# Kernel optimization log

Measured on AMD Instinct MI355X. Metric: run time of the kernel, lower is better.

Reference implementation:

```python
import jax, jax.numpy as jnp
import numpy as np

FIELD_DIMS = [256] * 8          # 8 fields, 2048 total features
N_FACTORS = 64
BATCH = 8192
INIT_STD = 0.01


def setup_inputs() -> dict:
    key = jax.random.key(0)
    k_x, k_v = jax.random.split(key)
    n_features = sum(FIELD_DIMS)
    n_fields = len(FIELD_DIMS)
    x = jax.random.normal(k_x, (BATCH, n_features), dtype=jnp.float32)
    # Parameters initialized as in FFMtorchNN.initialize()
    b = jnp.zeros((1,), dtype=jnp.float32)
    w = jnp.zeros((n_features, 1), dtype=jnp.float32)
    V = INIT_STD * jax.random.normal(k_v, (n_features, n_fields, N_FACTORS), dtype=jnp.float32)
    # feat2field[i] = field index of feature i
    feat2field = jnp.asarray(np.repeat(np.arange(n_fields), FIELD_DIMS), dtype=jnp.int32)
    return {"x": x, "b": b, "w": w, "V": V, "feat2field": feat2field}


def reference(x, b, w, V, feat2field):
    # Linear term: sum(x @ w, dim=1) -> [B]
    total_linear = (x @ w)[:, 0]

    n_fields = V.shape[1]
    # One-hot field membership of each feature: E [F, n_fields]
    E = jax.nn.one_hot(feat2field, n_fields, dtype=x.dtype)
    # M[b, s, t, l] = sum_{i in field s} x[b,i] * V[i, t, l]
    M = jnp.einsum('bi,is,itl->bstl', x, E, V)

    # Full ordered-pair bilinear sum: sum_{i,j} x_i x_j <V[i, f(j)], V[j, f(i)]>
    full = jnp.einsum('bstl,btsl->b', M, M)
    # Self terms (i == j): x_i^2 * ||V[i, f(i)]||^2
    V_self = jnp.take_along_axis(V, feat2field[:, None, None].astype(jnp.int32), axis=1)[:, 0, :]  # [F, L]
    q = jnp.einsum('bi,i->b', x * x, jnp.sum(V_self * V_self, axis=-1))

    # Original: total_inter = sum_{i<j} 0.5 * <t_i, t_j>  ==  0.25 * (full - q)
    total_inter = 0.25 * (full - q)

    y_pred = b[0] + total_linear + total_inter  # [B]
    return y_pred
```

## Files before the change

kernel.cpp:

```cpp
#include <hip/hip_runtime.h>

#define BATCH  8192
#define NFEAT  2048
#define NFIELD 8
#define NFACT  64
#define FDIM   256
#define NPAIR  36

typedef short short8v __attribute__((ext_vector_type(8)));
typedef __bf16 bf16x8 __attribute__((ext_vector_type(8)));
typedef float f32x4 __attribute__((ext_vector_type(4)));

__device__ inline unsigned short f2bf(float f) {
    unsigned int u = __float_as_uint(f);
    unsigned int r = u + 0x7FFF + ((u >> 16) & 1);
    return (unsigned short)(r >> 16);
}
__device__ inline float bf2f(unsigned short h) {
    return __uint_as_float(((unsigned int)h) << 16);
}
__device__ inline f32x4 mfma16(bf16x8 a, bf16x8 b, f32x4 c) {
    return __builtin_amdgcn_mfma_f32_16x16x32_bf16(a, b, c, 0, 0, 0);
}

__global__ void sv_kernel(const float* __restrict__ V, const int* __restrict__ f2f,
                          float* __restrict__ sv) {
    int i = blockIdx.x * blockDim.x + threadIdx.x;
    if (i >= NFEAT) return;
    int f = f2f[i];
    const float* vp = V + (size_t)i * (NFIELD * NFACT) + (size_t)f * NFACT;
    float s = 0.f;
#pragma unroll
    for (int l = 0; l < NFACT; l += 4) {
        float4 v = *reinterpret_cast<const float4*>(vp + l);
        s += v.x * v.x + v.y * v.y + v.z * v.z + v.w * v.w;
    }
    sv[i] = s;
}

__global__ void init_out(const float* __restrict__ bptr, float* __restrict__ out) {
    int i = blockIdx.x * blockDim.x + threadIdx.x;
    if (i < BATCH) out[i] = bptr[0];
}

__global__ void convert_v(const float* __restrict__ V,
                          unsigned short* __restrict__ vh, unsigned short* __restrict__ vl) {
    const int tid = blockIdx.x * 256 + threadIdx.x;
    const int lane = tid & 63;
    const int ct = (tid >> 6) & 3;
    const int kc = (tid >> 8) & 7;
    const int t  = (tid >> 11) & 7;
    const int s  = tid >> 14;
    const int l  = ct * 16 + (lane & 15);
    const int i0 = s * 256 + kc * 32 + (lane >> 4) * 8;
    short8v hv, lv;
#pragma unroll
    for (int e = 0; e < 8; ++e) {
        float v = V[(size_t)(i0 + e) * (NFIELD * NFACT) + t * NFACT + l];
        unsigned short h = f2bf(v);
        hv[e] = (short)h;
        lv[e] = (short)f2bf(v - bf2f(h));
    }
    *reinterpret_cast<short8v*>(vh + (size_t)tid * 8) = hv;
    *reinterpret_cast<short8v*>(vl + (size_t)tid * 8) = lv;
}

__global__ __launch_bounds__(256) void convert_x3(
    const float* __restrict__ x, const float* __restrict__ w,
    const float* __restrict__ sv,
    unsigned short* __restrict__ xh, unsigned short* __restrict__ xl,
    float* __restrict__ out) {
    __shared__ float tile[16][260];

    const int bid = blockIdx.x;
    const int rb  = bid >> 6;
    const int rt  = (bid >> 3) & 7;
    const int s   = bid & 7;
    const int row0 = rb * 128 + rt * 16;

    const int tid  = threadIdx.x;
    const int lane = tid & 63;
    const int wv   = tid >> 6;

    const int col = s * 256 + lane * 4;
    float4 w4  = *reinterpret_cast<const float4*>(w + col);
    float4 sv4 = *reinterpret_cast<const float4*>(sv + col);

    float lq[4];
#pragma unroll
    for (int p = 0; p < 4; ++p) {
        const int r = wv * 4 + p;
        float4 v = *reinterpret_cast<const float4*>(
            x + (size_t)(row0 + r) * NFEAT + col);
        *reinterpret_cast<float4*>(&tile[r][lane * 4]) = v;
        float lin = v.x * w4.x + v.y * w4.y + v.z * w4.z + v.w * w4.w;
        float q   = v.x * v.x * sv4.x + v.y * v.y * sv4.y
                  + v.z * v.z * sv4.z + v.w * v.w * sv4.w;
        lq[p] = lin - 0.25f * q;
    }
#pragma unroll
    for (int off = 1; off < 64; off <<= 1)
#pragma unroll
        for (int p = 0; p < 4; ++p)
            lq[p] += __shfl_xor(lq[p], off, 64);
    if (lane == 0) {
#pragma unroll
        for (int p = 0; p < 4; ++p)
            atomicAdd(&out[row0 + wv * 4 + p], lq[p]);
    }

    __syncthreads();

#pragma unroll
    for (int half = 0; half < 2; ++half) {
        const int kc = half * 4 + wv;
        const int r  = lane & 15;
        const int k0 = kc * 32 + (lane >> 4) * 8;
        float4 a = *reinterpret_cast<const float4*>(&tile[r][k0]);
        float4 b = *reinterpret_cast<const float4*>(&tile[r][k0 + 4]);
        float vs[8] = {a.x, a.y, a.z, a.w, b.x, b.y, b.z, b.w};
        short8v hv, lv;
#pragma unroll
        for (int e = 0; e < 8; ++e) {
            unsigned short h = f2bf(vs[e]);
            hv[e] = (short)h;
            lv[e] = (short)f2bf(vs[e] - bf2f(h));
        }
        size_t off = ((((size_t)(rb * 8 + s) * 8 + kc) * 8 + rt) * 64 + lane) * 8;
        *reinterpret_cast<short8v*>(xh + off) = hv;
        *reinterpret_cast<short8v*>(xl + off) = lv;
    }
}

__global__ __launch_bounds__(256, 3) void pair_mfma3(
    const unsigned short* __restrict__ xh, const unsigned short* __restrict__ xl,
    const unsigned short* __restrict__ vh, const unsigned short* __restrict__ vl,
    float* __restrict__ out) {
    __shared__ unsigned short lds[24576];

    const int id    = blockIdx.x;
    const int local = id >> 3;
    const int tile  = (id & 7) * 8 + local / 36;
    int p = local % 36;
    int s = 0;
    while (p >= NFIELD - s) { p -= NFIELD - s; ++s; }
    const int t = s + p;
    const bool diag = (s == t);

    const int tid = threadIdx.x, lane = tid & 63, wid = tid >> 6;
    const int rt0 = wid * 2, rt1 = rt0 + 1;

    f32x4 accA[2][4] = {};
    f32x4 accB[2][4] = {};

    const unsigned short* xsrc = (wid & 1) ? xl : xh;
    const unsigned short* vsrc = (wid & 1) ? vl : vh;
    const int f     = (wid < 2) ? s : t;
    const int vpair = (wid < 2) ? (s * 8 + t) : (t * 8 + s);
    const int xdst  = wid * 4096;
    const int vdst  = 16384 + wid * 2048;
    const bool active = !(diag && wid >= 2);

    const size_t xbase = ((size_t)(tile * 8 + f) * 8) * 4096 + (size_t)lane * 8;
    const size_t vbase = ((size_t)(vpair * 8)) * 2048 + (size_t)lane * 8;

    short8v xr[8], vr[4];
    if (active) {
#pragma unroll
        for (int rt = 0; rt < 8; ++rt)
            xr[rt] = *reinterpret_cast<const short8v*>(xsrc + xbase + rt * 512);
#pragma unroll
        for (int ct = 0; ct < 4; ++ct)
            vr[ct] = *reinterpret_cast<const short8v*>(vsrc + vbase + ct * 512);
    }

    for (int kc = 0; kc < 8; ++kc) {
        __syncthreads();
        if (active) {
#pragma unroll
            for (int rt = 0; rt < 8; ++rt)
                *reinterpret_cast<short8v*>(&lds[xdst + rt * 512 + lane * 8]) = xr[rt];
#pragma unroll
            for (int ct = 0; ct < 4; ++ct)
                *reinterpret_cast<short8v*>(&lds[vdst + ct * 512 + lane * 8]) = vr[ct];
        }
        __syncthreads();

        if (kc < 7 && active) {
            const size_t xo = xbase + (size_t)(kc + 1) * 4096;
            const size_t vo = vbase + (size_t)(kc + 1) * 2048;
#pragma unroll
            for (int rt = 0; rt < 8; ++rt)
                xr[rt] = *reinterpret_cast<const short8v*>(xsrc + xo + rt * 512);
#pragma unroll
            for (int ct = 0; ct < 4; ++ct)
                vr[ct] = *reinterpret_cast<const short8v*>(vsrc + vo + ct * 512);
        }

        bf16x8 ah0 = *reinterpret_cast<const bf16x8*>(&lds[0     + rt0 * 512 + lane * 8]);
        bf16x8 ah1 = *reinterpret_cast<const bf16x8*>(&lds[0     + rt1 * 512 + lane * 8]);
        bf16x8 al0 = *reinterpret_cast<const bf16x8*>(&lds[4096  + rt0 * 512 + lane * 8]);
        bf16x8 al1 = *reinterpret_cast<const bf16x8*>(&lds[4096  + rt1 * 512 + lane * 8]);
#pragma unroll
        for (int ct = 0; ct < 4; ++ct) {
            bf16x8 bh = *reinterpret_cast<const bf16x8*>(&lds[16384 + ct * 512 + lane * 8]);
            bf16x8 bl = *reinterpret_cast<const bf16x8*>(&lds[18432 + ct * 512 + lane * 8]);
            accA[0][ct] = mfma16(ah0, bh, accA[0][ct]);
            accA[0][ct] = mfma16(ah0, bl, accA[0][ct]);
            accA[0][ct] = mfma16(al0, bh, accA[0][ct]);
            accA[1][ct] = mfma16(ah1, bh, accA[1][ct]);
            accA[1][ct] = mfma16(ah1, bl, accA[1][ct]);
            accA[1][ct] = mfma16(al1, bh, accA[1][ct]);
        }
        if (!diag) {
            bf16x8 ch0 = *reinterpret_cast<const bf16x8*>(&lds[8192  + rt0 * 512 + lane * 8]);
            bf16x8 ch1 = *reinterpret_cast<const bf16x8*>(&lds[8192  + rt1 * 512 + lane * 8]);
            bf16x8 cl0 = *reinterpret_cast<const bf16x8*>(&lds[12288 + rt0 * 512 + lane * 8]);
            bf16x8 cl1 = *reinterpret_cast<const bf16x8*>(&lds[12288 + rt1 * 512 + lane * 8]);
#pragma unroll
            for (int ct = 0; ct < 4; ++ct) {
                bf16x8 bh = *reinterpret_cast<const bf16x8*>(&lds[20480 + ct * 512 + lane * 8]);
                bf16x8 bl = *reinterpret_cast<const bf16x8*>(&lds[22528 + ct * 512 + lane * 8]);
                accB[0][ct] = mfma16(ch0, bh, accB[0][ct]);
                accB[0][ct] = mfma16(ch0, bl, accB[0][ct]);
                accB[0][ct] = mfma16(cl0, bh, accB[0][ct]);
                accB[1][ct] = mfma16(ch1, bh, accB[1][ct]);
                accB[1][ct] = mfma16(ch1, bl, accB[1][ct]);
                accB[1][ct] = mfma16(cl1, bh, accB[1][ct]);
            }
        }
    }

    const float scale = diag ? 0.25f : 0.5f;
#pragma unroll
    for (int rti = 0; rti < 2; ++rti) {
#pragma unroll
        for (int r = 0; r < 4; ++r) {
            float v = 0.f;
#pragma unroll
            for (int ct = 0; ct < 4; ++ct)
                v += accA[rti][ct][r] * (diag ? accA[rti][ct][r] : accB[rti][ct][r]);
            v += __shfl_xor(v, 1, 64);
            v += __shfl_xor(v, 2, 64);
            v += __shfl_xor(v, 4, 64);
            v += __shfl_xor(v, 8, 64);
            if ((lane & 15) == 0) {
                int row = tile * 128 + (wid * 2 + rti) * 16 + (lane >> 4) * 4 + r;
                atomicAdd(&out[row], scale * v);
            }
        }
    }
}

#define BM 64
#define KC 64
#define XPAD 4

__global__ void base_kernel(const float* __restrict__ x, const float* __restrict__ bptr,
                            const float* __restrict__ w, const float* __restrict__ sv,
                            float* __restrict__ out) {
    const int row = blockIdx.x;
    const int tid = threadIdx.x;
    const float* xr = x + (size_t)row * NFEAT;
    float lin = 0.f, q = 0.f;
#pragma unroll
    for (int j = 0; j < 2; ++j) {
        int idx = j * 1024 + tid * 4;
        float4 xv = *reinterpret_cast<const float4*>(xr + idx);
        float4 wv = *reinterpret_cast<const float4*>(w + idx);
        float4 sq = *reinterpret_cast<const float4*>(sv + idx);
        lin += xv.x * wv.x + xv.y * wv.y + xv.z * wv.z + xv.w * wv.w;
        q   += xv.x * xv.x * sq.x + xv.y * xv.y * sq.y
             + xv.z * xv.z * sq.z + xv.w * xv.w * sq.w;
    }
#pragma unroll
    for (int off = 32; off >= 1; off >>= 1) {
        lin += __shfl_down(lin, off, 64);
        q   += __shfl_down(q, off, 64);
    }
    __shared__ float slin[4], sq4[4];
    const int wave = tid >> 6;
    if ((tid & 63) == 0) { slin[wave] = lin; sq4[wave] = q; }
    __syncthreads();
    if (tid == 0) {
        float L = slin[0] + slin[1] + slin[2] + slin[3];
        float Q = sq4[0] + sq4[1] + sq4[2] + sq4[3];
        out[row] = bptr[0] + L - 0.25f * Q;
    }
}

__global__ __launch_bounds__(256) void pair_kernel(const float* __restrict__ x,
                                                   const float* __restrict__ V,
                                                   float* __restrict__ out) {
    __shared__ float Xs[BM][KC + XPAD];
    __shared__ float Xt[BM][KC + XPAD];
    __shared__ float Vs[KC][NFACT];
    __shared__ float Vt[KC][NFACT];

    const int tile = blockIdx.x;
    int p = blockIdx.y;
    int s = 0;
    while (p >= NFIELD - s) { p -= NFIELD - s; ++s; }
    const int t = s + p;
    const bool diag = (s == t);

    const int tid  = threadIdx.x;
    const int lgrp = tid & 15;
    const int rgrp = tid >> 4;
    const int l0 = lgrp * 4;
    const int r0 = rgrp * 4;
    const int rowBase = tile * BM;

    float accA[4][4] = {};
    float accB[4][4] = {};

    for (int kc = 0; kc < FDIM; kc += KC) {
        __syncthreads();
#pragma unroll
        for (int it = 0; it < 4; ++it) {
            int rr = (tid >> 4) + it * 16;
            const float* gx = x + (size_t)(rowBase + rr) * NFEAT + s * FDIM + kc + (tid & 15) * 4;
            *reinterpret_cast<float4*>(&Xs[rr][(tid & 15) * 4]) =
                *reinterpret_cast<const float4*>(gx);
            if (!diag) {
                const float* gx2 = x + (size_t)(rowBase + rr) * NFEAT + t * FDIM + kc + (tid & 15) * 4;
                *reinterpret_cast<float4*>(&Xt[rr][(tid & 15) * 4]) =
                    *reinterpret_cast<const float4*>(gx2);
            }
        }
#pragma unroll
        for (int it = 0; it < 4; ++it) {
            int kk = (tid >> 4) + it * 16;
            const float* gv = V + (size_t)(s * FDIM + kc + kk) * (NFIELD * NFACT) + t * NFACT + (tid & 15) * 4;
            *reinterpret_cast<float4*>(&Vs[kk][(tid & 15) * 4]) =
                *reinterpret_cast<const float4*>(gv);
            if (!diag) {
                const float* gv2 = V + (size_t)(t * FDIM + kc + kk) * (NFIELD * NFACT) + s * NFACT + (tid & 15) * 4;
                *reinterpret_cast<float4*>(&Vt[kk][(tid & 15) * 4]) =
                    *reinterpret_cast<const float4*>(gv2);
            }
        }
        __syncthreads();

        for (int k = 0; k < KC; k += 4) {
            float xa[4][4], va[4][4];
#pragma unroll
            for (int r = 0; r < 4; ++r) {
                float4 v = *reinterpret_cast<const float4*>(&Xs[r0 + r][k]);
                xa[r][0] = v.x; xa[r][1] = v.y; xa[r][2] = v.z; xa[r][3] = v.w;
            }
#pragma unroll
            for (int kk = 0; kk < 4; ++kk) {
                float4 v = *reinterpret_cast<const float4*>(&Vs[k + kk][l0]);
                va[kk][0] = v.x; va[kk][1] = v.y; va[kk][2] = v.z; va[kk][3] = v.w;
            }
#pragma unroll
            for (int kk = 0; kk < 4; ++kk)
#pragma unroll
                for (int r = 0; r < 4; ++r)
#pragma unroll
                    for (int c = 0; c < 4; ++c)
                        accA[r][c] = fmaf(xa[r][kk], va[kk][c], accA[r][c]);

            if (!diag) {
                float xb[4][4], vb[4][4];
#pragma unroll
                for (int r = 0; r < 4; ++r) {
                    float4 v = *reinterpret_cast<const float4*>(&Xt[r0 + r][k]);
                    xb[r][0] = v.x; xb[r][1] = v.y; xb[r][2] = v.z; xb[r][3] = v.w;
                }
#pragma unroll
                for (int kk = 0; kk < 4; ++kk) {
                    float4 v = *reinterpret_cast<const float4*>(&Vt[k + kk][l0]);
                    vb[kk][0] = v.x; vb[kk][1] = v.y; vb[kk][2] = v.z; vb[kk][3] = v.w;
                }
#pragma unroll
                for (int kk = 0; kk < 4; ++kk)
#pragma unroll
                    for (int r = 0; r < 4; ++r)
#pragma unroll
                        for (int c = 0; c < 4; ++c)
                            accB[r][c] = fmaf(xb[r][kk], vb[kk][c], accB[r][c]);
            }
        }
    }

    float pr[4];
#pragma unroll
    for (int r = 0; r < 4; ++r) {
        float d = 0.f;
#pragma unroll
        for (int c = 0; c < 4; ++c)
            d += accA[r][c] * (diag ? accA[r][c] : accB[r][c]);
        pr[r] = d;
    }
#pragma unroll
    for (int off = 1; off < 16; off <<= 1) {
#pragma unroll
        for (int r = 0; r < 4; ++r)
            pr[r] += __shfl_xor(pr[r], off, 64);
    }
    if (lgrp == 0) {
        const float scale = diag ? 0.25f : 0.5f;
#pragma unroll
        for (int r = 0; r < 4; ++r)
            atomicAdd(&out[rowBase + r0 + r], scale * pr[r]);
    }
}

extern "C" void kernel_launch(void* const* d_in, const int* in_sizes, int n_in,
                              void* d_out, int out_size, void* d_ws, size_t ws_size,
                              hipStream_t stream) {
    const float* x   = (const float*)d_in[0];
    const float* b   = (const float*)d_in[1];
    const float* w   = (const float*)d_in[2];
    const float* V   = (const float*)d_in[3];
    const int*   f2f = (const int*)d_in[4];
    float* out = (float*)d_out;

    const size_t SZ_XH = 33554432;
    const size_t SZ_VH = 2097152;
    const size_t NEED  = 2 * SZ_XH + 2 * SZ_VH + NFEAT * sizeof(float);

    if (ws_size >= NEED) {
        char* ws = (char*)d_ws;
        unsigned short* xhp = (unsigned short*)ws;
        unsigned short* xlp = (unsigned short*)(ws + SZ_XH);
        unsigned short* vhp = (unsigned short*)(ws + 2 * SZ_XH);
        unsigned short* vlp = (unsigned short*)(ws + 2 * SZ_XH + SZ_VH);
        float* sv = (float*)(ws + 2 * SZ_XH + 2 * SZ_VH);

        sv_kernel<<<(NFEAT + 255) / 256, 256, 0, stream>>>(V, f2f, sv);
        init_out<<<(BATCH + 255) / 256, 256, 0, stream>>>(b, out);
        convert_v<<<131072 / 256, 256, 0, stream>>>(V, vhp, vlp);
        convert_x3<<<4096, 256, 0, stream>>>(x, w, sv, xhp, xlp, out);
        pair_mfma3<<<64 * NPAIR, 256, 0, stream>>>(xhp, xlp, vhp, vlp, out);
    } else {
        float* sv = (float*)d_ws;
        sv_kernel<<<(NFEAT + 255) / 256, 256, 0, stream>>>(V, f2f, sv);
        base_kernel<<<BATCH, 256, 0, stream>>>(x, b, w, sv, out);
        dim3 grid(BATCH / BM, NPAIR);
        pair_kernel<<<grid, 256, 0, stream>>>(x, V, out);
    }
}
```

Baseline: 178.9 us.

## Load X fragments directly into registers and double-buffer only V in LDS

Reworks the pair MFMA kernel so each wave loads its X row fragments (hi/lo) straight from global memory into registers instead of staging them through shared memory, and only the V tiles go through a double-buffered LDS buffer. Waves now split output into a 2x2 grid over row tiles and column tiles rather than taking row tiles only. This cuts LDS traffic and footprint and drops one barrier per k-step. In exchange, X fragments are read from global memory twice (once per column-half wave), register pressure rises, and global load latency is exposed because X is not prefetched.

```diff
diff --git a/kernel.cpp b/kernel.cpp
--- a/kernel.cpp
+++ b/kernel.cpp
@@ -132,11 +132,11 @@
     }
 }
 
-__global__ __launch_bounds__(256, 3) void pair_mfma3(
+__global__ __launch_bounds__(256, 3) void pair_mfma4(
     const unsigned short* __restrict__ xh, const unsigned short* __restrict__ xl,
     const unsigned short* __restrict__ vh, const unsigned short* __restrict__ vl,
     float* __restrict__ out) {
-    __shared__ unsigned short lds[24576];
+    __shared__ unsigned short vbuf[2][4][2048];
 
     const int id    = blockIdx.x;
     const int local = id >> 3;
@@ -148,104 +148,105 @@
     const bool diag = (s == t);
 
     const int tid = threadIdx.x, lane = tid & 63, wid = tid >> 6;
-    const int rt0 = wid * 2, rt1 = rt0 + 1;
-
-    f32x4 accA[2][4] = {};
-    f32x4 accB[2][4] = {};
-
-    const unsigned short* xsrc = (wid & 1) ? xl : xh;
+    const int rh = wid >> 1;
+    const int ch = wid & 1;
+
+    f32x4 accA[4][2] = {};
+    f32x4 accB[4][2] = {};
+
     const unsigned short* vsrc = (wid & 1) ? vl : vh;
-    const int f     = (wid < 2) ? s : t;
     const int vpair = (wid < 2) ? (s * 8 + t) : (t * 8 + s);
-    const int xdst  = wid * 4096;
-    const int vdst  = 16384 + wid * 2048;
-    const bool active = !(diag && wid >= 2);
-
-    const size_t xbase = ((size_t)(tile * 8 + f) * 8) * 4096 + (size_t)lane * 8;
-    const size_t vbase = ((size_t)(vpair * 8)) * 2048 + (size_t)lane * 8;
-
-    short8v xr[8], vr[4];
-    if (active) {
-#pragma unroll
-        for (int rt = 0; rt < 8; ++rt)
-            xr[rt] = *reinterpret_cast<const short8v*>(xsrc + xbase + rt * 512);
-#pragma unroll
-        for (int ct = 0; ct < 4; ++ct)
-            vr[ct] = *reinterpret_cast<const short8v*>(vsrc + vbase + ct * 512);
+    const bool vactive = !(diag && wid >= 2);
+    const size_t vbase = (size_t)vpair * 8 * 2048 + (size_t)(lane * 8);
+
+    const size_t xbaseS = (size_t)(tile * 8 + s) * 8 * 4096
+                        + (size_t)((rh * 4) * 512 + lane * 8);
+    const size_t xbaseT = (size_t)(tile * 8 + t) * 8 * 4096
+                        + (size_t)((rh * 4) * 512 + lane * 8);
+
+    if (vactive) {
+        short8v vr[4];
+#pragma unroll
+        for (int i = 0; i < 4; ++i)
+            vr[i] = *reinterpret_cast<const short8v*>(vsrc + vbase + i * 512);
+#pragma unroll
+        for (int i = 0; i < 4; ++i)
+            *reinterpret_cast<short8v*>(&vbuf[0][wid][i * 512 + lane * 8]) = vr[i];
     }
 
     for (int kc = 0; kc < 8; ++kc) {
+        const int cur = kc & 1;
+        const size_t xoS = xbaseS + (size_t)kc * 4096;
+        const size_t xoT = xbaseT + (size_t)kc * 4096;
+
+        bf16x8 xah[4], xal[4], xch[4], xcl[4];
+#pragma unroll
+        for (int i = 0; i < 4; ++i) {
+            xah[i] = *reinterpret_cast<const bf16x8*>(xh + xoS + i * 512);
+            xal[i] = *reinterpret_cast<const bf16x8*>(xl + xoS + i * 512);
+        }
+        if (!diag) {
+#pragma unroll
+            for (int i = 0; i < 4; ++i) {
+                xch[i] = *reinterpret_cast<const bf16x8*>(xh + xoT + i * 512);
+                xcl[i] = *reinterpret_cast<const bf16x8*>(xl + xoT + i * 512);
+            }
+        }
+        short8v vn[4];
+        if (kc < 7 && vactive) {
+            const size_t vo = vbase + (size_t)(kc + 1) * 2048;
+#pragma unroll
+            for (int i = 0; i < 4; ++i)
+                vn[i] = *reinterpret_cast<const short8v*>(vsrc + vo + i * 512);
+        }
+
         __syncthreads();
-        if (active) {
-#pragma unroll
-            for (int rt = 0; rt < 8; ++rt)
-                *reinterpret_cast<short8v*>(&lds[xdst + rt * 512 + lane * 8]) = xr[rt];
-#pragma unroll
-            for (int ct = 0; ct < 4; ++ct)
-                *reinterpret_cast<short8v*>(&lds[vdst + ct * 512 + lane * 8]) = vr[ct];
-        }
-        __syncthreads();
-
-        if (kc < 7 && active) {
-            const size_t xo = xbase + (size_t)(kc + 1) * 4096;
-            const size_t vo = vbase + (size_t)(kc + 1) * 2048;
-#pragma unroll
-            for (int rt = 0; rt < 8; ++rt)
-                xr[rt] = *reinterpret_cast<const short8v*>(xsrc + xo + rt * 512);
-#pragma unroll
-            for (int ct = 0; ct < 4; ++ct)
-                vr[ct] = *reinterpret_cast<const short8v*>(vsrc + vo + ct * 512);
-        }
-
-        bf16x8 ah0 = *reinterpret_cast<const bf16x8*>(&lds[0     + rt0 * 512 + lane * 8]);
-        bf16x8 ah1 = *reinterpret_cast<const bf16x8*>(&lds[0     + rt1 * 512 + lane * 8]);
-        bf16x8 al0 = *reinterpret_cast<const bf16x8*>(&lds[4096  + rt0 * 512 + lane * 8]);
-        bf16x8 al1 = *reinterpret_cast<const bf16x8*>(&lds[4096  + rt1 * 512 + lane * 8]);
-#pragma unroll
-        for (int ct = 0; ct < 4; ++ct) {
-            bf16x8 bh = *reinterpret_cast<const bf16x8*>(&lds[16384 + ct * 512 + lane * 8]);
-            bf16x8 bl = *reinterpret_cast<const bf16x8*>(&lds[18432 + ct * 512 + lane * 8]);
-            accA[0][ct] = mfma16(ah0, bh, accA[0][ct]);
-            accA[0][ct] = mfma16(ah0, bl, accA[0][ct]);
-            accA[0][ct] = mfma16(al0, bh, accA[0][ct]);
-            accA[1][ct] = mfma16(ah1, bh, accA[1][ct]);
-            accA[1][ct] = mfma16(ah1, bl, accA[1][ct]);
-            accA[1][ct] = mfma16(al1, bh, accA[1][ct]);
-        }
-        if (!diag) {
-            bf16x8 ch0 = *reinterpret_cast<const bf16x8*>(&lds[8192  + rt0 * 512 + lane * 8]);
-            bf16x8 ch1 = *reinterpret_cast<const bf16x8*>(&lds[8192  + rt1 * 512 + lane * 8]);
-            bf16x8 cl0 = *reinterpret_cast<const bf16x8*>(&lds[12288 + rt0 * 512 + lane * 8]);
-            bf16x8 cl1 = *reinterpret_cast<const bf16x8*>(&lds[12288 + rt1 * 512 + lane * 8]);
-#pragma unroll
-            for (int ct = 0; ct < 4; ++ct) {
-                bf16x8 bh = *reinterpret_cast<const bf16x8*>(&lds[20480 + ct * 512 + lane * 8]);
-                bf16x8 bl = *reinterpret_cast<const bf16x8*>(&lds[22528 + ct * 512 + lane * 8]);
-                accB[0][ct] = mfma16(ch0, bh, accB[0][ct]);
-                accB[0][ct] = mfma16(ch0, bl, accB[0][ct]);
-                accB[0][ct] = mfma16(cl0, bh, accB[0][ct]);
-                accB[1][ct] = mfma16(ch1, bh, accB[1][ct]);
-                accB[1][ct] = mfma16(ch1, bl, accB[1][ct]);
-                accB[1][ct] = mfma16(cl1, bh, accB[1][ct]);
-            }
+
+#pragma unroll
+        for (int j = 0; j < 2; ++j) {
+            const int ct = ch * 2 + j;
+            bf16x8 bh = *reinterpret_cast<const bf16x8*>(&vbuf[cur][0][ct * 512 + lane * 8]);
+            bf16x8 bl = *reinterpret_cast<const bf16x8*>(&vbuf[cur][1][ct * 512 + lane * 8]);
+#pragma unroll
+            for (int i = 0; i < 4; ++i) {
+                accA[i][j] = mfma16(xah[i], bh, accA[i][j]);
+                accA[i][j] = mfma16(xah[i], bl, accA[i][j]);
+                accA[i][j] = mfma16(xal[i], bh, accA[i][j]);
+            }
+            if (!diag) {
+                bf16x8 dh = *reinterpret_cast<const bf16x8*>(&vbuf[cur][2][ct * 512 + lane * 8]);
+                bf16x8 dl = *reinterpret_cast<const bf16x8*>(&vbuf[cur][3][ct * 512 + lane * 8]);
+#pragma unroll
+                for (int i = 0; i < 4; ++i) {
+                    accB[i][j] = mfma16(xch[i], dh, accB[i][j]);
+                    accB[i][j] = mfma16(xch[i], dl, accB[i][j]);
+                    accB[i][j] = mfma16(xcl[i], dh, accB[i][j]);
+                }
+            }
+        }
+
+        if (kc < 7 && vactive) {
+#pragma unroll
+            for (int i = 0; i < 4; ++i)
+                *reinterpret_cast<short8v*>(&vbuf[cur ^ 1][wid][i * 512 + lane * 8]) = vn[i];
         }
     }
 
     const float scale = diag ? 0.25f : 0.5f;
 #pragma unroll
-    for (int rti = 0; rti < 2; ++rti) {
+    for (int i = 0; i < 4; ++i) {
 #pragma unroll
         for (int r = 0; r < 4; ++r) {
             float v = 0.f;
 #pragma unroll
-            for (int ct = 0; ct < 4; ++ct)
-                v += accA[rti][ct][r] * (diag ? accA[rti][ct][r] : accB[rti][ct][r]);
+            for (int j = 0; j < 2; ++j)
+                v += accA[i][j][r] * (diag ? accA[i][j][r] : accB[i][j][r]);
             v += __shfl_xor(v, 1, 64);
             v += __shfl_xor(v, 2, 64);
             v += __shfl_xor(v, 4, 64);
             v += __shfl_xor(v, 8, 64);
             if ((lane & 15) == 0) {
-                int row = tile * 128 + (wid * 2 + rti) * 16 + (lane >> 4) * 4 + r;
+                int row = tile * 128 + (rh * 4 + i) * 16 + (lane >> 4) * 4 + r;
                 atomicAdd(&out[row], scale * v);
             }
         }
@@ -434,7 +435,7 @@
         init_out<<<(BATCH + 255) / 256, 256, 0, stream>>>(b, out);
         convert_v<<<131072 / 256, 256, 0, stream>>>(V, vhp, vlp);
         convert_x3<<<4096, 256, 0, stream>>>(x, w, sv, xhp, xlp, out);
-        pair_mfma3<<<64 * NPAIR, 256, 0, stream>>>(xhp, xlp, vhp, vlp, out);
+        pair_mfma4<<<64 * NPAIR, 256, 0, stream>>>(xhp, xlp, vhp, vlp, out);
     } else {
         float* sv = (float*)d_ws;
         sv_kernel<<<(NFEAT + 255) / 256, 256, 0, stream>>>(V, f2f, sv);
```

New measurement: 235.3 us. 31.5% more time.
